# Optimization experiments

Measured on AMD Instinct MI355X. Metric: run time of the kernel, lower is better.

The kernel has to match this reference:

```python
import jax, jax.numpy as jnp
import numpy as np

V_TH = 1.0    # LIF threshold
V_RESET = 0.0 # LIF reset value
DECAY = 0.3   # LIF decay factor


def _xavier_uniform(key, shape):
    # shape = (fan_out, fan_in) like torch Linear weight
    fan_out, fan_in = shape
    bound = float(np.sqrt(6.0 / (fan_in + fan_out)))
    return jax.random.uniform(key, shape, jnp.float32, -bound, bound)


def setup_inputs() -> dict:
    key = jax.random.key(0)
    k_x, k_win, k_wout, k_bout = jax.random.split(key, 4)
    B, C, H, W = 512, 3, 32, 32
    input_size = C * H * W      # 3072
    hidden_size = 2048
    output_size = 512
    x = jax.random.normal(k_x, (B, C, H, W), jnp.float32)
    W_in = _xavier_uniform(k_win, (hidden_size, input_size))
    W_out = _xavier_uniform(k_wout, (output_size, hidden_size))
    b_out = jnp.zeros((output_size,), jnp.float32)
    return {"x": x, "W_in": W_in, "W_out": W_out, "b_out": b_out, "T": 10}


def reference(x, W_in, W_out, b_out, T):
    B = x.shape[0]
    xf = x.reshape(B, -1)                       # [B, input_size]
    p = jax.nn.sigmoid(xf)                      # spike probability per pixel
    keys = jax.random.split(jax.random.key(42), T)
    hidden = W_in.shape[0]
    out_dim = W_out.shape[0]
    v0 = jnp.zeros((B, hidden), xf.dtype)
    s0 = jnp.zeros((B, out_dim), xf.dtype)

    def step(carry, k):
        v, s = carry
        u = jax.random.uniform(k, p.shape, p.dtype)
        pre = (u < p).astype(p.dtype)           # stochastic input spikes [B, input]
        h = pre @ W_in.T                        # [B, hidden]
        v = v * DECAY + h                       # LIF decay + integrate
        spikes = (v >= V_TH).astype(p.dtype)    # fire
        v = jnp.where(spikes > 0, V_RESET, v)   # reset fired neurons
        out = spikes @ W_out.T + b_out          # [B, out]
        s = s + (out > 0).astype(p.dtype)       # output spike count
        return (v, s), None

    (v, s), _ = jax.lax.scan(step, (v0, s0), keys)
    return s
```

## Files before the change

kernel.cpp:

```cpp
#include <hip/hip_runtime.h>
#include <cstdint>

#define B_SZ   512
#define IN_SZ  3072
#define HID    2048
#define OUT_SZ 512
#define T_STEPS 10
#define NELEM  (512u*3072u)
#define KW     96
#define BITS_T_STRIDE (512u*96u)
#define M_ALL  (T_STEPS * B_SZ)
#define SCALE_UP   16384.0f
#define SCALE_DN   6.103515625e-05f

typedef __attribute__((ext_vector_type(8))) _Float16 half8;
typedef __attribute__((ext_vector_type(4))) float f32x4;
typedef __attribute__((ext_vector_type(16))) float f32x16;
typedef __attribute__((ext_vector_type(4))) unsigned int u32x4;

struct Keys { uint32_t k[2*T_STEPS]; };

__host__ __device__ inline void threefry2x32(uint32_t k0, uint32_t k1,
                                             uint32_t x0, uint32_t x1,
                                             uint32_t& y0, uint32_t& y1) {
  const uint32_t ks2 = k0 ^ k1 ^ 0x1BD11BDAu;
#define TF_R(r) { x0 += x1; x1 = (x1 << (r)) | (x1 >> (32-(r))); x1 ^= x0; }
  x0 += k0; x1 += k1;
  TF_R(13) TF_R(15) TF_R(26) TF_R(6)   x0 += k1;  x1 += ks2 + 1u;
  TF_R(17) TF_R(29) TF_R(16) TF_R(24)  x0 += ks2; x1 += k0  + 2u;
  TF_R(13) TF_R(15) TF_R(26) TF_R(6)   x0 += k0;  x1 += k1  + 3u;
  TF_R(17) TF_R(29) TF_R(16) TF_R(24)  x0 += k1;  x1 += ks2 + 4u;
  TF_R(13) TF_R(15) TF_R(26) TF_R(6)   x0 += ks2; x1 += k0  + 5u;
#undef TF_R
  y0 = x0; y1 = x1;
}

__device__ __forceinline__ void split2x8h(const float* __restrict__ src,
                                          half8& hv, half8& mv) {
  float w8[8];
  *(f32x4*)&w8[0] = *(const f32x4*)&src[0];
  *(f32x4*)&w8[4] = *(const f32x4*)&src[4];
  union { _Float16 f[8]; half8 v; } h8, m8;
#pragma unroll
  for (int j = 0; j < 8; ++j) {
    float ws = w8[j] * SCALE_UP;
    _Float16 h = (_Float16)ws;
    float r1 = ws - (float)h;
    _Float16 m = (_Float16)r1;
    h8.f[j] = h; m8.f[j] = m;
  }
  hv = h8.v; mv = m8.v;
}

__device__ __forceinline__ half8 expand8h(uint32_t b) {
  union { uint32_t u[4]; half8 v; } r;
#pragma unroll
  for (int j = 0; j < 4; ++j) {
    uint32_t x = b >> (2*j);
    r.u[j] = ((x & 1u) | ((x & 2u) << 15)) * 0x3C00u;
  }
  return r.v;
}

__global__ __launch_bounds__(256) void prep_kernel(
    const float* __restrict__ x, const float* __restrict__ Win,
    const float* __restrict__ Wout,
    ushort* __restrict__ Wfrag, ushort* __restrict__ Ofrag,
    uint32_t* __restrict__ pre_bits, Keys keys) {
  int blk = blockIdx.x;
  int tid = threadIdx.x;
  if (blk < 3072) {
    int bx = blk % 48, nt = blk / 48;
    int col = tid & 31;
    int cell = tid >> 5;
    int ks = bx * 4 + (cell >> 1);
    int kh = cell & 1;
    half8 hv, mv;
    split2x8h(&Win[(size_t)(nt * 32 + col) * IN_SZ + ks * 16 + kh * 8],
              hv, mv);
    size_t base =
        ((size_t)nt * (IN_SZ / 16) + ks) * 1024 + (kh * 32 + col) * 8;
    *(half8*)&Wfrag[base]       = hv;
    *(half8*)&Wfrag[base + 512] = mv;
  } else if (blk < 3584) {
    int q = blk - 3072;
    int bx = q % 16, nt = q / 16;
    int ks = bx * 4 + (tid >> 6);
    int kb = (tid >> 4) & 3, c = tid & 15;
    half8 hv, mv;
    split2x8h(&Wout[(size_t)(nt * 16 + c) * HID + ks * 32 + kb * 8], hv, mv);
    size_t base =
        ((size_t)nt * (HID / 32) + ks) * 1024 + (kb * 16 + c) * 8;
    *(half8*)&Ofrag[base]       = hv;
    *(half8*)&Ofrag[base + 512] = mv;
  } else {
    uint32_t m = (uint32_t)(blk - 3584) * 256u + tid;
    uint32_t b = m / IN_SZ;
    uint32_t j = m - b * IN_SZ;
    float xv = x[m];
    float p = (float)(1.0 / (1.0 + exp(-(double)xv)));
    uint32_t lane = tid & 63u;
    uint32_t wbase = b * KW + (j >> 5);
#pragma unroll
    for (int t = 0; t < T_STEPS; ++t) {
      uint32_t y0, y1;
      threefry2x32(keys.k[2*t], keys.k[2*t+1], 0u, m, y0, y1);
      uint32_t bits = y0 ^ y1;
      float u = __uint_as_float((bits >> 9) | 0x3f800000u) - 1.0f;
      unsigned long long mask = __ballot(u < p);
      if (lane == 0u) {
        *reinterpret_cast<unsigned long long*>(
            &pre_bits[(uint32_t)t * BITS_T_STRIDE + wbase]) = mask;
      }
    }
  }
}

#define MFMAH(a, b, c)   __builtin_amdgcn_mfma_f32_16x16x32_f16((a), (b), (c), 0, 0, 0)
#define MFMAH32(a, b, c) __builtin_amdgcn_mfma_f32_32x32x16_f16((a), (b), (c), 0, 0, 0)

__global__ __launch_bounds__(256) void gemm_hidden(
    const ushort* __restrict__ Wfrag,
    const uint32_t* __restrict__ in_bits,
    float* __restrict__ H) {
  __shared__ ushort A_lds[2][10240];
  int lin = blockIdx.x;
  int xcd = lin & 7, w = lin >> 3;
  int xb  = xcd * 2 + (w >> 5);
  int mb  = w & 31;
  int tid  = threadIdx.x;
  int wave = tid >> 6, lane = tid & 63;
  int col  = lane & 31, kh = lane >> 5;
  int nt = xb * 4 + wave;
  int m0 = mb * 160;
  const ushort* bp = Wfrag + (size_t)nt * (192 * 1024);

  int s0 = tid * 5;
  int r0 = s0 >> 3, r1 = (s0 + 4) >> 3;
  const uint32_t* rowp0 = in_bits + (size_t)(m0 + r0) * KW;
  const uint32_t* rowp1 = in_bits + (size_t)(m0 + r1) * KW;
  int hi_[5], ws_[5], sh_[5], off_[5];
#pragma unroll
  for (int p = 0; p < 5; ++p) {
    int s = s0 + p, r = s >> 3, j = s & 7;
    hi_[p]  = (r != r0);
    ws_[p]  = (j >> 2) & 1;
    sh_[p]  = (j & 3) * 8;
    off_[p] = (j * 5 + (r >> 5)) * 256 + (r & 31) * 8;
  }

  f32x16 acc[5];
#pragma unroll
  for (int f = 0; f < 5; ++f)
#pragma unroll
    for (int r = 0; r < 16; ++r) acc[f][r] = 0.f;

  uint2 br0, br1;

#define STAGE(buf)                                                            \
  {                                                                           \
    _Pragma("unroll")                                                         \
    for (int p = 0; p < 5; ++p) {                                             \
      uint32_t wv = hi_[p] ? (ws_[p] ? br1.y : br1.x)                         \
                           : (ws_[p] ? br0.y : br0.x);                        \
      *(half8*)&A_lds[buf][off_[p]] = expand8h((wv >> sh_[p]) & 0xFFu);       \
    }                                                                         \
  }

#define BURST(sidx)                                                           \
  {                                                                           \
    int g2 = kc * 4 + (sidx) + 2;                                             \
    if (g2 > 191) g2 = 191;                                                   \
    const ushort* bn = bp + (size_t)g2 * 1024 + lane * 8;                     \
    half8 Bn0 = *(const half8*)&bn[0];                                        \
    half8 Bn1 = *(const half8*)&bn[512];                                      \
    half8 A[5];                                                               \
    _Pragma("unroll")                                                         \
    for (int f = 0; f < 5; ++f)                                               \
      A[f] = *(const half8*)&A_lds[cur][(sidx) * 2560 + aoff + f * 256];      \
    __builtin_amdgcn_s_setprio(1);                                            \
    _Pragma("unroll")                                                         \
    for (int f = 0; f < 5; ++f) acc[f] = MFMAH32(A[f], Bc0, acc[f]);          \
    _Pragma("unroll")                                                         \
    for (int f = 0; f < 5; ++f) acc[f] = MFMAH32(A[f], Bc1, acc[f]);          \
    __builtin_amdgcn_s_setprio(0);                                            \
    Bc0 = Bd0; Bc1 = Bd1;                                                     \
    Bd0 = Bn0; Bd1 = Bn1;                                                     \
  }

  br0 = *(const uint2*)&rowp0[0];
  br1 = *(const uint2*)&rowp1[0];
  STAGE(0)
  br0 = *(const uint2*)&rowp0[2];
  br1 = *(const uint2*)&rowp1[2];
  half8 Bc0, Bc1, Bd0, Bd1;
  {
    const ushort* bk = bp + lane * 8;
    Bc0 = *(const half8*)&bk[0];
    Bc1 = *(const half8*)&bk[512];
    const ushort* bd = bk + 1024;
    Bd0 = *(const half8*)&bd[0];
    Bd1 = *(const half8*)&bd[512];
  }
  __syncthreads();

  int aoff = kh * 5 * 256 + col * 8;

  for (int kc = 0; kc < 48; ++kc) {
    int cur = kc & 1;
    BURST(0)
    if (kc + 1 < 48) STAGE(cur ^ 1)
    if (kc + 2 < 48) {
      br0 = *(const uint2*)&rowp0[(kc + 2) * 2];
      br1 = *(const uint2*)&rowp1[(kc + 2) * 2];
    }
    BURST(1)
    BURST(2)
    BURST(3)
    __syncthreads();
  }
#undef BURST
#undef STAGE

#pragma unroll
  for (int f = 0; f < 5; ++f)
#pragma unroll
    for (int r = 0; r < 16; ++r) {
      int m = m0 + f * 32 + (r & 3) + 8 * (r >> 2) + 4 * kh;
      H[(size_t)m * HID + nt * 32 + col] = acc[f][r] * SCALE_DN;
    }
}

__global__ __launch_bounds__(256) void lif_scan(
    const float* __restrict__ H,
    uint8_t* __restrict__ spk) {
  int idx  = blockIdx.x * 256 + threadIdx.x;
  int b = idx >> 11, n = idx & 2047;
  int lane = threadIdx.x & 63;
  size_t spk_off = (size_t)b * 256 + (size_t)((n >> 3) & ~7);
  float v = 0.f;
#pragma unroll
  for (int t = 0; t < T_STEPS; ++t) {
    float h = H[(size_t)(t * B_SZ + b) * HID + n];
    bool fire;
    {
#pragma clang fp contract(off)
      float vd = v * 0.3f;
      float vn = vd + h;
      fire = (vn >= 1.0f);
      v = fire ? 0.0f : vn;
    }
    unsigned long long mask = __ballot(fire);
    if (lane == 0)
      *(unsigned long long*)&spk[(size_t)t * (512*256) + spk_off] = mask;
  }
}

__global__ __launch_bounds__(256) void out_mfma(
    const ushort* __restrict__ Ofrag,
    const uint8_t* __restrict__ spk,
    const float* __restrict__ bout,
    float* __restrict__ s) {
  int lin = blockIdx.x;
  int x = lin & 7;
  int r0 = lin >> 3;
  int y = r0 & 7;
  int t = r0 >> 3;
  int tid = threadIdx.x;
  int wave = tid >> 6, lane = tid & 63;
  int col  = lane & 15, kb = lane >> 4;
  int nt = x * 4 + wave;
  int m0 = y * 64;
  const ushort* bp = Ofrag + (size_t)nt * (64 * 1024);
  const uint8_t* st = spk + (size_t)t * (512*256);

  f32x4 acc[4] = {{0.f,0.f,0.f,0.f},{0.f,0.f,0.f,0.f},
                  {0.f,0.f,0.f,0.f},{0.f,0.f,0.f,0.f}};

  u32x4 aw[4], awn[4];
#pragma unroll
  for (int f = 0; f < 4; ++f)
    aw[f] = *(const u32x4*)&st[(size_t)(m0 + f*16 + col) * 256];
  half8 Bc0, Bc1;
  {
    const ushort* bk = bp + lane * 8;
    Bc0 = *(const half8*)&bk[0];
    Bc1 = *(const half8*)&bk[512];
  }

  for (int kc4 = 0; kc4 < 16; ++kc4) {
    int nk4 = (kc4 + 1 < 16) ? kc4 + 1 : 15;
#pragma unroll
    for (int f = 0; f < 4; ++f)
      awn[f] = *(const u32x4*)&st[(size_t)(m0 + f*16 + col) * 256 + nk4*16];
#pragma unroll
    for (int sv = 0; sv < 4; ++sv) {
      int g1 = kc4 * 4 + sv + 1;
      if (g1 > 63) g1 = 63;
      const ushort* bn = bp + (size_t)g1 * 1024 + lane * 8;
      half8 Bn0 = *(const half8*)&bn[0];
      half8 Bn1 = *(const half8*)&bn[512];
      half8 A[4];
#pragma unroll
      for (int f = 0; f < 4; ++f)
        A[f] = expand8h((aw[f][sv] >> (kb*8)) & 0xFFu);
      __builtin_amdgcn_s_setprio(1);
#pragma unroll
      for (int f = 0; f < 4; ++f) acc[f] = MFMAH(A[f], Bc0, acc[f]);
#pragma unroll
      for (int f = 0; f < 4; ++f) acc[f] = MFMAH(A[f], Bc1, acc[f]);
      __builtin_amdgcn_s_setprio(0);
      Bc0 = Bn0; Bc1 = Bn1;
    }
#pragma unroll
    for (int f = 0; f < 4; ++f) aw[f] = awn[f];
  }
  float bo = bout[nt*16 + col];
#pragma unroll
  for (int f = 0; f < 4; ++f) {
#pragma unroll
    for (int r = 0; r < 4; ++r) {
      float out = acc[f][r] * SCALE_DN + bo;
      if (out > 0.0f) {
        int b = m0 + f*16 + kb*4 + r;
        atomicAdd(&s[(size_t)b * OUT_SZ + nt*16 + col], 1.0f);
      }
    }
  }
}

extern "C" void kernel_launch(void* const* d_in, const int* in_sizes, int n_in,
                              void* d_out, int out_size, void* d_ws, size_t ws_size,
                              hipStream_t stream) {
  const float* x    = (const float*)d_in[0];
  const float* Win  = (const float*)d_in[1];
  const float* Wout = (const float*)d_in[2];
  const float* bout = (const float*)d_in[3];
  float* s = (float*)d_out;

  char* ws = (char*)d_ws;
  ushort*   Wfrag   = (ushort*)(ws + 0);
  ushort*   Ofrag   = (ushort*)(ws + 25165824);
  uint32_t* in_bits = (uint32_t*)(ws + 29360128);
  uint8_t*  spk     = (uint8_t*)(ws + 31326208);
  float*    H       = (float*)(ws + 32636928);

  Keys hk;
  for (int t = 0; t < T_STEPS; ++t) {
    uint32_t y0, y1;
    threefry2x32(0u, 42u, 0u, (uint32_t)t, y0, y1);
    hk.k[2*t] = y0; hk.k[2*t+1] = y1;
  }

  (void)hipMemsetAsync(d_out, 0, (size_t)OUT_SZ * B_SZ * sizeof(float), stream);
  hipLaunchKernelGGL(prep_kernel, dim3(3072 + 512 + NELEM/256), dim3(256), 0,
                     stream, x, Win, Wout, Wfrag, Ofrag, in_bits, hk);
  hipLaunchKernelGGL(gemm_hidden, dim3(512), dim3(256), 0, stream,
                     Wfrag, in_bits, H);
  hipLaunchKernelGGL(lif_scan, dim3((B_SZ*HID)/256), dim3(256), 0, stream,
                     H, spk);
  hipLaunchKernelGGL(out_mfma, dim3(8 * 8 * T_STEPS), dim3(256), 0, stream,
                     Ofrag, spk, bout, s);
}
```

Baseline: 214.4 us.

## Fuse LIF scan into hidden GEMM epilogue with batch-major time interleaving

Reorders the input spike bit layout so the 10 time steps of each batch row sit next to each other, letting each GEMM tile of 160 rows cover 16 batch rows across all time steps. The LIF recurrence then runs in the GEMM epilogue from LDS, and the spike masks are written directly, removing the fp32 H round trip through global memory and the separate lif_scan launch. The cost is extra LDS staging passes and barriers in the GEMM tail.

Measured after the change: 207.0 us. -3.5%, faster.

```diff
diff --git a/kernel.cpp b/kernel.cpp
--- a/kernel.cpp
+++ b/kernel.cpp
@@ -8,7 +8,6 @@
 #define T_STEPS 10
 #define NELEM  (512u*3072u)
 #define KW     96
-#define BITS_T_STRIDE (512u*96u)
 #define M_ALL  (T_STEPS * B_SZ)
 #define SCALE_UP   16384.0f
 #define SCALE_DN   6.103515625e-05f
@@ -100,7 +99,6 @@
     float xv = x[m];
     float p = (float)(1.0 / (1.0 + exp(-(double)xv)));
     uint32_t lane = tid & 63u;
-    uint32_t wbase = b * KW + (j >> 5);
 #pragma unroll
     for (int t = 0; t < T_STEPS; ++t) {
       uint32_t y0, y1;
@@ -110,7 +108,7 @@
       unsigned long long mask = __ballot(u < p);
       if (lane == 0u) {
         *reinterpret_cast<unsigned long long*>(
-            &pre_bits[(uint32_t)t * BITS_T_STRIDE + wbase]) = mask;
+            &pre_bits[(b * 10u + (uint32_t)t) * KW + (j >> 5)]) = mask;
       }
     }
   }
@@ -122,7 +120,7 @@
 __global__ __launch_bounds__(256) void gemm_hidden(
     const ushort* __restrict__ Wfrag,
     const uint32_t* __restrict__ in_bits,
-    float* __restrict__ H) {
+    uint8_t* __restrict__ spk) {
   __shared__ ushort A_lds[2][10240];
   int lin = blockIdx.x;
   int xcd = lin & 7, w = lin >> 3;
@@ -222,37 +220,45 @@
 #undef BURST
 #undef STAGE
 
-#pragma unroll
-  for (int f = 0; f < 5; ++f)
-#pragma unroll
-    for (int r = 0; r < 16; ++r) {
-      int m = m0 + f * 32 + (r & 3) + 8 * (r >> 2) + 4 * kh;
-      H[(size_t)m * HID + nt * 32 + col] = acc[f][r] * SCALE_DN;
-    }
-}
-
-__global__ __launch_bounds__(256) void lif_scan(
-    const float* __restrict__ H,
-    uint8_t* __restrict__ spk) {
-  int idx  = blockIdx.x * 256 + threadIdx.x;
-  int b = idx >> 11, n = idx & 2047;
-  int lane = threadIdx.x & 63;
-  size_t spk_off = (size_t)b * 256 + (size_t)((n >> 3) & ~7);
-  float v = 0.f;
-#pragma unroll
-  for (int t = 0; t < T_STEPS; ++t) {
-    float h = H[(size_t)(t * B_SZ + b) * HID + n];
-    bool fire;
-    {
+  float* h_lds = (float*)&A_lds[0][0];
+  int lcol = wave * 32 + col;
+#pragma unroll
+  for (int ph = 0; ph < 2; ++ph) {
+    __syncthreads();
+    if ((lcol >> 6) == ph) {
+      int lc = lcol & 63;
+#pragma unroll
+      for (int f = 0; f < 5; ++f)
+#pragma unroll
+        for (int r = 0; r < 16; ++r) {
+          int lr = f * 32 + (r & 3) + 8 * (r >> 2) + 4 * kh;
+          h_lds[lr * 64 + lc] = acc[f][r] * SCALE_DN;
+        }
+    }
+    __syncthreads();
+    int nbyte0 = xb * 16 + ph * 8;
+#pragma unroll
+    for (int i = 0; i < 4; ++i) {
+      int lb = wave * 4 + i;
+      int b = mb * 16 + lb;
+      float v = 0.f;
+#pragma unroll
+      for (int t = 0; t < T_STEPS; ++t) {
+        float h = h_lds[(lb * 10 + t) * 64 + lane];
+        bool fire;
+        {
 #pragma clang fp contract(off)
-      float vd = v * 0.3f;
-      float vn = vd + h;
-      fire = (vn >= 1.0f);
-      v = fire ? 0.0f : vn;
-    }
-    unsigned long long mask = __ballot(fire);
-    if (lane == 0)
-      *(unsigned long long*)&spk[(size_t)t * (512*256) + spk_off] = mask;
+          float vd = v * 0.3f;
+          float vn = vd + h;
+          fire = (vn >= 1.0f);
+          v = fire ? 0.0f : vn;
+        }
+        unsigned long long mask = __ballot(fire);
+        if (lane == 0)
+          *(unsigned long long*)&spk[(size_t)t * (512*256) +
+                                     (size_t)b * 256 + nbyte0] = mask;
+      }
+    }
   }
 }
 
@@ -343,7 +349,6 @@
   ushort*   Ofrag   = (ushort*)(ws + 25165824);
   uint32_t* in_bits = (uint32_t*)(ws + 29360128);
   uint8_t*  spk     = (uint8_t*)(ws + 31326208);
-  float*    H       = (float*)(ws + 32636928);
 
   Keys hk;
   for (int t = 0; t < T_STEPS; ++t) {
@@ -356,9 +361,7 @@
   hipLaunchKernelGGL(prep_kernel, dim3(3072 + 512 + NELEM/256), dim3(256), 0,
                      stream, x, Win, Wout, Wfrag, Ofrag, in_bits, hk);
   hipLaunchKernelGGL(gemm_hidden, dim3(512), dim3(256), 0, stream,
-                     Wfrag, in_bits, H);
-  hipLaunchKernelGGL(lif_scan, dim3((B_SZ*HID)/256), dim3(256), 0, stream,
-                     H, spk);
+                     Wfrag, in_bits, spk);
   hipLaunchKernelGGL(out_mfma, dim3(8 * 8 * T_STEPS), dim3(256), 0, stream,
                      Ofrag, spk, bout, s);
 }
```
